# Kernel optimization log

Hardware: AMD Instinct MI355X
Metric: run time of the kernel (lower is better)

The kernel has to match this reference:

```python
import jax, jax.numpy as jnp
import numpy as np
import math

S_SLOTS = 8
DS = 256
ITERS = 3
SIGMA = 5.0
L = 6        # fourier frequencies
FB = 2.0     # freq base
SCALE = DS ** -0.5


def ln(x, g, b, eps=1e-5):
    m = x.mean(-1, keepdims=True)
    v = ((x - m) ** 2).mean(-1, keepdims=True)
    return (x - m) / jnp.sqrt(v + eps) * g + b


def fourier(c):
    # c: (..., 3) -> (..., 3 + 2*3*L), layout [coords, interleaved (sin,cos) per (dim,freq)]
    freqs = FB ** jnp.arange(L, dtype=c.dtype)
    sc = c[..., None] * freqs * (2.0 * math.pi)            # (..., 3, L)
    ff = jnp.stack([jnp.sin(sc), jnp.cos(sc)], axis=-1)    # (..., 3, L, 2)
    ff = ff.reshape(*c.shape[:-1], -1)
    return jnp.concatenate([c, ff], axis=-1)


def n2n(x):
    return jnp.nan_to_num(x, nan=0.0, posinf=1.0, neginf=-1.0)


def gru_cell(x, h, wih, whh, bih, bhh):
    gi = x @ wih.T + bih
    gh = h @ whh.T + bhh
    ir, iz, inn = jnp.split(gi, 3, axis=-1)
    hr, hz, hn = jnp.split(gh, 3, axis=-1)
    r = jax.nn.sigmoid(ir + hr)
    z = jax.nn.sigmoid(iz + hz)
    n = jnp.tanh(inn + r * hn)
    return (1.0 - z) * n + z * h


def isa_forward(inputs, coords, slots_p, Ss0, Sp0, Qw, Kw, Vw, gw, gb,
                f1w, f1b, f2w, f2b, ng, nb, wih, whh, bih, bhh,
                m_ng, m_nb, m1w, m1b, m2w, m2b,
                i0g, i0b, i1w, i1b, i2w, i2b, i3g, i3b, fw, fb):
    B, N, D = inputs.shape
    eps = 1e-8
    slots = jnp.broadcast_to(slots_p, (B, S_SLOTS, DS))
    slots_init = slots
    # initial_mlp: LN -> Linear -> ReLU -> Linear -> LN
    x = ln(inputs, i0g, i0b)
    x = jax.nn.relu(x @ i1w.T + i1b)
    x = x @ i2w.T + i2b
    x = ln(x, i3g, i3b)
    x = n2n(x)                              # (B, N, DS)
    Kx = x @ Kw.T                           # (B, N, DS) (same for every slot)
    Vx = x @ Vw.T
    abs_grid = coords[:, None]              # (B, 1, N, 3)
    S_p = jnp.broadcast_to(Sp0, (B, S_SLOTS, 1, 3))
    S_s = jnp.broadcast_to(Ss0, (B, S_SLOTS, 1, 3))

    def f_mlp(t):
        return jax.nn.relu(t @ f1w.T + f1b) @ f2w.T + f2b

    attn = None
    for t in range(ITERS + 1):
        if t == ITERS - 1:  # query_opt straight-through trick
            slots = jax.lax.stop_gradient(slots) + slots_init - jax.lax.stop_gradient(slots_init)
        slots_prev = slots
        sn = ln(slots, ng, nb)
        Ss_safe = jnp.clip(S_s, 0.3, 5.0) + 0.1
        rel = jnp.clip((abs_grid - S_p) / (Ss_safe * SIGMA + 1e-4), -3.0, 3.0)  # (B,S,N,3)
        gr = fourier(rel) @ gw.T + gb                                           # (B,S,N,DS)
        k = f_mlp(Kx[:, None] + gr)
        v = f_mlp(Vx[:, None] + gr)
        q = sn @ Qw.T                                                           # (B,S,DS)
        dots = jnp.clip(jnp.einsum('bsd,bsnd->bsn', q, k) * SCALE, -30.0, 30.0)
        attn = jax.nn.softmax(dots, axis=1) + eps          # softmax over slots
        attn = attn / (attn.sum(-1, keepdims=True) + eps)  # normalize over points
        updates = jnp.einsum('bsnd,bsn->bsd', v, attn)
        S_p = jnp.einsum('bnd,bsn->bsd', coords, attn)[:, :, None]              # (B,S,1,3)
        diff2 = (abs_grid - S_p) ** 2
        S_s = jnp.clip(jnp.sqrt(jnp.einsum('bsnd,bsn->bsd', diff2, attn) + 1e-6), 0.2, 5.0)[:, :, None]
        if t != ITERS:
            upd = n2n(updates).reshape(-1, DS)
            slots = gru_cell(upd, slots_prev.reshape(-1, DS), wih, whh, bih, bhh).reshape(B, S_SLOTS, DS)
            # pre-norm residual MLP (dropout is identity in eval)
            h = ln(slots, m_ng, m_nb)
            slots = slots + (jax.nn.relu(h @ m1w.T + m1b) @ m2w.T + m2b)
            slots = n2n(slots)
    out_slots = slots_prev @ fw.T + fb
    return out_slots, attn


def setup_inputs() -> dict:
    key = jax.random.key(0)
    ks = iter(jax.random.split(key, 64))
    B, N, D = 4, 2048, 768
    CENC = 3 + 2 * 3 * L  # 39

    def rn(shape, s=0.05):
        return (jax.random.normal(next(ks), shape, jnp.float32) * s)

    d = dict(
        inputs=jax.random.normal(next(ks), (B, N, D), jnp.float32),
        coords=jax.random.uniform(next(ks), (B, N, 3), jnp.float32),
        slots_p=rn((1, S_SLOTS, DS)),
        Ss0=0.5 + 0.1 * jax.random.normal(next(ks), (1, S_SLOTS, 1, 3), jnp.float32),
        Sp0=0.02 * jax.random.normal(next(ks), (1, S_SLOTS, 1, 3), jnp.float32),
        Qw=rn((DS, DS)), Kw=rn((DS, DS)), Vw=rn((DS, DS)),
        gw=rn((DS, CENC)), gb=jnp.zeros((DS,), jnp.float32),
        f1w=rn((DS, DS)), f1b=jnp.zeros((DS,), jnp.float32),
        f2w=rn((DS, DS)), f2b=jnp.zeros((DS,), jnp.float32),
        ng=jnp.ones((DS,), jnp.float32), nb=jnp.zeros((DS,), jnp.float32),
        wih=rn((3 * DS, DS)), whh=rn((3 * DS, DS)),
        bih=jnp.zeros((3 * DS,), jnp.float32), bhh=jnp.zeros((3 * DS,), jnp.float32),
        m_ng=jnp.ones((DS,), jnp.float32), m_nb=jnp.zeros((DS,), jnp.float32),
        m1w=rn((4 * DS, DS)), m1b=jnp.zeros((4 * DS,), jnp.float32),
        m2w=rn((DS, 4 * DS)), m2b=jnp.zeros((DS,), jnp.float32),
        i0g=jnp.ones((D,), jnp.float32), i0b=jnp.zeros((D,), jnp.float32),
        i1w=rn((D, D), 0.03), i1b=jnp.zeros((D,), jnp.float32),
        i2w=rn((DS, D), 0.03), i2b=jnp.zeros((DS,), jnp.float32),
        i3g=jnp.ones((DS,), jnp.float32), i3b=jnp.zeros((DS,), jnp.float32),
        fw=rn((DS, DS)), fb=jnp.zeros((DS,), jnp.float32),
    )
    return d


def reference(inputs, coords, slots_p, Ss0, Sp0, Qw, Kw, Vw, gw, gb,
              f1w, f1b, f2w, f2b, ng, nb, wih, whh, bih, bhh,
              m_ng, m_nb, m1w, m1b, m2w, m2b,
              i0g, i0b, i1w, i1b, i2w, i2b, i3g, i3b, fw, fb):
    return isa_forward(inputs, coords, slots_p, Ss0, Sp0, Qw, Kw, Vw, gw, gb,
                       f1w, f1b, f2w, f2b, ng, nb, wih, whh, bih, bhh,
                       m_ng, m_nb, m1w, m1b, m2w, m2b,
                       i0g, i0b, i1w, i1b, i2w, i2b, i3g, i3b, fw, fb)
```

## Files before the change

kernel.cpp:

```cpp
#include <hip/hip_runtime.h>
#include <math.h>

#define DEVI __device__ __forceinline__

typedef __attribute__((ext_vector_type(8))) short short8;
typedef __attribute__((ext_vector_type(4))) float f32x4;

DEVI float bf2f(short u){ unsigned v = ((unsigned)(unsigned short)u) << 16; return __builtin_bit_cast(float, v); }
DEVI short f2bs(float f){
  unsigned x = __builtin_bit_cast(unsigned, f);
  unsigned r = (x + 0x7fffu + ((x >> 16) & 1u)) >> 16;
  return (short)(unsigned short)r;
}
DEVI float clampf(float x, float lo, float hi){ return fminf(fmaxf(x, lo), hi); }
DEVI float n2nf(float x){
  if (x != x) return 0.f;
  if (x == INFINITY) return 1.f;
  if (x == -INFINITY) return -1.f;
  return x;
}
DEVI float sigmoidf(float x){ return 1.f/(1.f+expf(-x)); }
DEVI f32x4 mfma16(short8 a, short8 b, f32x4 c){ return __builtin_amdgcn_mfma_f32_16x16x32_bf16(a,b,c,0,0,0); }

DEVI float blkSum(float v, float* s4, int tid){
  #pragma unroll
  for (int o=32;o;o>>=1) v += __shfl_xor(v,o);
  __syncthreads();
  if ((tid&63)==0) s4[tid>>6] = v;
  __syncthreads();
  return s4[0]+s4[1]+s4[2]+s4[3];
}

DEVI float ffval(int c, float r0, float r1, float r2){
  if (c >= 40) return 0.f;
  if (c == 39) return 1.f;
  if (c < 3) return (c==0)?r0:((c==1)?r1:r2);
  int q = c-3, i = q/12, j = (q%12)>>1;
  float ri = (i==0)?r0:((i==1)?r1:r2);
  float ang = ri * (6.283185307179586f * (float)(1u<<j));
  return (q&1) ? __cosf(ang) : __sinf(ang);
}

DEVI void qprep_body(float sl, int bs, int t,
    const float* __restrict__ ng, const float* __restrict__ nbv, const float* __restrict__ Qw,
    const float* __restrict__ f2w, const float* __restrict__ f2b,
    float* __restrict__ qf2, float* __restrict__ qbv,
    float* sn, float* q, float* s4){
  float m = blkSum(sl, s4, t)*(1.f/256.f);
  float d = sl - m;
  float var = blkSum(d*d, s4, t)*(1.f/256.f);
  sn[t] = d*(1.f/sqrtf(var+1e-5f))*ng[t] + nbv[t];
  __syncthreads();
  {
    const float4* qr = (const float4*)(Qw + (size_t)t*256);
    float s = 0.f;
    for (int d4=0; d4<64; ++d4){
      float4 w4 = qr[d4];
      s += sn[d4*4+0]*w4.x + sn[d4*4+1]*w4.y + sn[d4*4+2]*w4.z + sn[d4*4+3]*w4.w;
    }
    q[t] = s;
  }
  __syncthreads();
  {
    float s = 0.f;
    for (int o=0;o<256;o++) s += q[o]*f2w[(size_t)o*256 + t];
    qf2[bs*256+t] = s;
  }
  float tot = blkSum(q[t]*f2b[t], s4, t);
  if (t==0) qbv[bs] = tot;
}

__global__ void k_pack_w(const float* __restrict__ W, short* __restrict__ out, int KT, int total){
  int o = blockIdx.x*256 + threadIdx.x;
  if (o >= total) return;
  int l = o & 63;
  int frag = o >> 6;
  int KTt = KT >> 5;
  int ci = frag / KTt, kk = frag - ci*KTt;
  int col = ci*16 + (l & 15);
  int k0 = kk*32 + (l >> 4)*8;
  const float* src = W + (size_t)col*KT + k0;
  short8 v;
  #pragma unroll
  for (int e=0;e<8;e++) v[e] = f2bs(src[e]);
  *(short8*)(out + (size_t)o*8) = v;
}

__global__ void k_pack_gw(const float* __restrict__ gw, const float* __restrict__ gb, short* __restrict__ out){
  int o = blockIdx.x*256 + threadIdx.x;
  int l = o & 63;
  int frag = o >> 6;
  int ci = frag >> 1, kk = frag & 1;
  int col = ci*16 + (l&15);
  int k0 = kk*32 + (l>>4)*8;
  short8 v;
  #pragma unroll
  for (int e=0;e<8;e++){
    int c = k0 + e;
    float x = (c < 39) ? gw[col*39 + c] : (c == 39 ? gb[col] : 0.f);
    v[e] = f2bs(x);
  }
  *(short8*)(out + (size_t)o*8) = v;
}

__global__ __launch_bounds__(256) void k_init(const float* __restrict__ slots_p, const float* __restrict__ Sp0,
                       const float* __restrict__ Ss0,
                       float* __restrict__ slots, float* __restrict__ sp, float* __restrict__ ssb,
                       const float* __restrict__ ng, const float* __restrict__ nbv, const float* __restrict__ Qw,
                       const float* __restrict__ f2w, const float* __restrict__ f2b,
                       float* __restrict__ qf2, float* __restrict__ qbv){
  int bs = blockIdx.x, t = threadIdx.x, s = bs & 7;
  __shared__ float sn[256], q[256], s4[4];
  float sl = slots_p[s*256+t];
  slots[bs*256+t] = sl;
  if (t < 3){ sp[bs*3+t] = Sp0[s*3+t]; ssb[bs*3+t] = Ss0[s*3+t]; }
  qprep_body(sl, bs, t, ng, nbv, Qw, f2w, f2b, qf2, qbv, sn, q, s4);
}

__global__ __launch_bounds__(256) void k_ln768(const float* __restrict__ in, const float* __restrict__ g,
                                               const float* __restrict__ bt, short* __restrict__ out){
  int r = blockIdx.x, t = threadIdx.x;
  __shared__ float s4[4];
  const float* row = in + (size_t)r*768;
  float x0=row[t], x1=row[256+t], x2=row[512+t];
  float m = blkSum(x0+x1+x2, s4, t) * (1.f/768.f);
  float d0=x0-m, d1=x1-m, d2=x2-m;
  float var = blkSum(d0*d0+d1*d1+d2*d2, s4, t) * (1.f/768.f);
  float rstd = 1.f/sqrtf(var + 1e-5f);
  short* orow = out + (size_t)r*768;
  orow[t]     = f2bs(d0*rstd*g[t]     + bt[t]);
  orow[256+t] = f2bs(d1*rstd*g[256+t] + bt[256+t]);
  orow[512+t] = f2bs(d2*rstd*g[512+t] + bt[512+t]);
}

__global__ __launch_bounds__(256) void k_ln256(const float* __restrict__ in, const float* __restrict__ g,
                                               const float* __restrict__ bt, short* __restrict__ out){
  int r = blockIdx.x, t = threadIdx.x;
  __shared__ float s4[4];
  float x = in[(size_t)r*256 + t];
  float m = blkSum(x, s4, t) * (1.f/256.f);
  float d = x - m;
  float var = blkSum(d*d, s4, t) * (1.f/256.f);
  out[(size_t)r*256 + t] = f2bs(d*(1.f/sqrtf(var+1e-5f))*g[t] + bt[t]);
}

__global__ __launch_bounds__(256) void k_gemm(const short* __restrict__ A, const short* __restrict__ Wp,
                                              const float* __restrict__ bias, void* __restrict__ outp,
                                              int ldo, int KT, int flags){
  const int w = threadIdx.x>>6, l = threadIdx.x&63, l15 = l&15, l4 = l>>4;
  const int row0 = blockIdx.x*64 + w*16;
  const int col0 = blockIdx.y*128;
  const int KTt = KT >> 5;
  f32x4 acc[8];
  #pragma unroll
  for (int i=0;i<8;i++) acc[i] = (f32x4)(0.f);
  const short* Ap = A + (size_t)(row0+l15)*KT + l4*8;
  #pragma unroll 2
  for (int kk=0; kk<KT/32; ++kk){
    short8 af = *(const short8*)(Ap + kk*32);
    #pragma unroll
    for (int ci=0; ci<8; ++ci){
      const short* bp = Wp + (((size_t)(blockIdx.y*8+ci)*KTt + kk)*64 + l)*8;
      acc[ci] = mfma16(af, *(const short8*)bp, acc[ci]);
    }
  }
  #pragma unroll
  for (int ci=0; ci<8; ++ci){
    int col = col0 + ci*16 + l15;
    float bv = (flags&1) ? bias[col] : 0.f;
    #pragma unroll
    for (int j=0;j<4;j++){
      int row = row0 + l4*4 + j;
      float v = acc[ci][j] + bv;
      if (flags&2) v = fmaxf(v, 0.f);
      if (flags&4) ((short*)outp)[(size_t)row*ldo + col] = f2bs(v);
      else         ((float*)outp)[(size_t)row*ldo + col] = v;
    }
  }
}

__global__ __launch_bounds__(256, 4) void k_isa_a(
    const float* __restrict__ coords, const float* __restrict__ sp, const float* __restrict__ ssb,
    const short* __restrict__ gwp, const short* __restrict__ kx, const short* __restrict__ vx,
    const short* __restrict__ f1wp, const float* __restrict__ f1b,
    const float* __restrict__ qf2, const float* __restrict__ qbv,
    float* __restrict__ dots, short* __restrict__ hv){
  __shared__ __align__(16) short abuf[64*256];
  __shared__ float sf1b[256];
  __shared__ float sqf2[256];
  __shared__ float smisc[8];
  const int tid = threadIdx.x;
  const int bs = blockIdx.y;
  const int b  = bs >> 3;
  const int n0 = blockIdx.x * 64;
  const int pass = blockIdx.z;

  sf1b[tid] = f1b[tid];
  sqf2[tid] = qf2[bs*256 + tid];
  if (tid < 3){
    smisc[tid] = sp[bs*3+tid];
    float sv = ssb[bs*3+tid];
    float sa = clampf(sv, 0.3f, 5.f) + 0.1f;
    smisc[4+tid] = 1.f/(sa*5.f + 1e-4f);
  }
  if (tid == 7) smisc[7] = qbv[bs];
  __syncthreads();

  const int w = tid>>6, l = tid&63, l15 = l&15, l4 = l>>4;
  const int ar = w*16 + l15;

  short8 ag0, ag1;
  {
    const float* cp0 = coords + ((size_t)(b*2048 + n0 + ar))*3;
    float r0 = clampf((cp0[0] - smisc[0]) * smisc[4], -3.f, 3.f);
    float r1 = clampf((cp0[1] - smisc[1]) * smisc[5], -3.f, 3.f);
    float r2 = clampf((cp0[2] - smisc[2]) * smisc[6], -3.f, 3.f);
    #pragma unroll
    for (int e=0;e<8;e++) ag0[e] = f2bs(ffval(l4*8+e,      r0,r1,r2));
    #pragma unroll
    for (int e=0;e<8;e++) ag1[e] = f2bs(ffval(32+l4*8+e,   r0,r1,r2));
  }

  #pragma unroll 2
  for (int cc=0; cc<8; ++cc){
    int f0 = (2*cc)*2, f1 = (2*cc+1)*2;
    f32x4 a0 = (f32x4)(0.f), a1 = (f32x4)(0.f);
    a0 = mfma16(ag0, *(const short8*)(gwp + ((size_t)(f0  )*64 + l)*8), a0);
    a0 = mfma16(ag1, *(const short8*)(gwp + ((size_t)(f0+1)*64 + l)*8), a0);
    a1 = mfma16(ag0, *(const short8*)(gwp + ((size_t)(f1  )*64 + l)*8), a1);
    a1 = mfma16(ag1, *(const short8*)(gwp + ((size_t)(f1+1)*64 + l)*8), a1);
    int c0 = (2*cc)*16 + l15, c1 = (2*cc+1)*16 + l15;
    #pragma unroll
    for (int j=0;j<4;j++){
      int row = w*16 + l4*4 + j;
      abuf[row*256 + (((c0>>3)^(row&7))<<3) + (c0&7)] = f2bs(a0[j]);
      abuf[row*256 + (((c1>>3)^(row&7))<<3) + (c1&7)] = f2bs(a1[j]);
    }
  }
  __syncthreads();
  {
    const short* srcb = pass ? vx : kx;
    #pragma unroll
    for (int i=0;i<8;i++){
      int gid = tid + i*256;
      int row = gid>>5, cg = gid&31;
      short8 sv = *(const short8*)(srcb + ((size_t)(b*2048 + n0 + row))*256 + cg*8);
      short* ap = &abuf[row*256 + ((cg^(row&7))<<3)];
      short8 av = *(const short8*)ap;
      short8 ov;
      #pragma unroll
      for (int e=0;e<8;e++) ov[e] = f2bs(bf2f(av[e]) + bf2f(sv[e]));
      *(short8*)ap = ov;
    }
  }
  __syncthreads();
  short8 af[8];
  #pragma unroll
  for (int kk=0;kk<8;kk++)
    af[kk] = *(const short8*)&abuf[ar*256 + (((kk*4+l4) ^ (ar&7))<<3)];

  if (pass == 0){
    float p0=0.f,p1=0.f,p2=0.f,p3=0.f;
    #pragma unroll 2
    for (int cc=0; cc<8; ++cc){
      int ct0 = 2*cc, ct1 = 2*cc+1;
      f32x4 a0 = (f32x4)(0.f), a1 = (f32x4)(0.f);
      #pragma unroll
      for (int kk=0;kk<8;kk++){
        a0 = mfma16(af[kk], *(const short8*)(f1wp + (((size_t)ct0*8 + kk)*64 + l)*8), a0);
        a1 = mfma16(af[kk], *(const short8*)(f1wp + (((size_t)ct1*8 + kk)*64 + l)*8), a1);
      }
      int c0 = ct0*16 + l15, c1 = ct1*16 + l15;
      float q0=sqf2[c0], b0=sf1b[c0], q1=sqf2[c1], b1=sf1b[c1];
      p0 += fmaxf(a0[0]+b0,0.f)*q0 + fmaxf(a1[0]+b1,0.f)*q1;
      p1 += fmaxf(a0[1]+b0,0.f)*q0 + fmaxf(a1[1]+b1,0.f)*q1;
      p2 += fmaxf(a0[2]+b0,0.f)*q0 + fmaxf(a1[2]+b1,0.f)*q1;
      p3 += fmaxf(a0[3]+b0,0.f)*q0 + fmaxf(a1[3]+b1,0.f)*q1;
    }
    #pragma unroll
    for (int o=8;o;o>>=1){
      p0 += __shfl_xor(p0,o); p1 += __shfl_xor(p1,o);
      p2 += __shfl_xor(p2,o); p3 += __shfl_xor(p3,o);
    }
    if (l15 == 0){
      float pj[4] = {p0,p1,p2,p3};
      #pragma unroll
      for (int j=0;j<4;j++){
        int row = w*16 + l4*4 + j;
        float dd = clampf((pj[j] + smisc[7]) * 0.0625f, -30.f, 30.f);
        dots[(size_t)bs*2048 + n0 + row] = dd;
      }
    }
  } else {
    #pragma unroll 2
    for (int cc=0; cc<8; ++cc){
      int ct0 = 2*cc, ct1 = 2*cc+1;
      f32x4 a0 = (f32x4)(0.f), a1 = (f32x4)(0.f);
      #pragma unroll
      for (int kk=0;kk<8;kk++){
        a0 = mfma16(af[kk], *(const short8*)(f1wp + (((size_t)ct0*8 + kk)*64 + l)*8), a0);
        a1 = mfma16(af[kk], *(const short8*)(f1wp + (((size_t)ct1*8 + kk)*64 + l)*8), a1);
      }
      int c0 = ct0*16 + l15, c1 = ct1*16 + l15;
      float b0=sf1b[c0], b1=sf1b[c1];
      #pragma unroll
      for (int j=0;j<4;j++){
        int row = w*16 + l4*4 + j;
        abuf[row*256 + (((c0>>3)^(row&7))<<3) + (c0&7)] = f2bs(fmaxf(a0[j]+b0,0.f));
        abuf[row*256 + (((c1>>3)^(row&7))<<3) + (c1&7)] = f2bs(fmaxf(a1[j]+b1,0.f));
      }
    }
    __syncthreads();
    #pragma unroll
    for (int i=0;i<8;i++){
      int gid = tid + i*256;
      int row = gid>>5, cg = gid&31;
      short8 av = *(const short8*)&abuf[row*256 + ((cg^(row&7))<<3)];
      *(short8*)(hv + ((size_t)(bs*2048 + n0 + row))*256 + cg*8) = av;
    }
  }
}

__global__ __launch_bounds__(256) void k_softmax(const float* __restrict__ dots, float* __restrict__ aun,
                                                 float* __restrict__ sump){
  int blk = blockIdx.x;
  int b = blk >> 3, chunk = blk & 7;
  int n = chunk*256 + threadIdx.x;
  float d[8];
  #pragma unroll
  for (int s=0;s<8;s++) d[s] = dots[(size_t)(b*8+s)*2048 + n];
  float m = d[0];
  #pragma unroll
  for (int s=1;s<8;s++) m = fmaxf(m, d[s]);
  float e[8]; float sum = 0.f;
  #pragma unroll
  for (int s=0;s<8;s++){ e[s] = expf(d[s]-m); sum += e[s]; }
  float inv = 1.f/sum;
  __shared__ float red[4][8];
  int wv = threadIdx.x>>6, ln = threadIdx.x&63;
  #pragma unroll
  for (int s=0;s<8;s++){
    float a = e[s]*inv + 1e-8f;
    aun[(size_t)(b*8+s)*2048 + n] = a;
    float v = a;
    #pragma unroll
    for (int o=32;o;o>>=1) v += __shfl_xor(v,o);
    if (ln == 0) red[wv][s] = v;
  }
  __syncthreads();
  if (threadIdx.x < 8){
    int s = threadIdx.x;
    sump[(b*8+s)*8 + chunk] = red[0][s]+red[1][s]+red[2][s]+red[3][s];
  }
}

__global__ __launch_bounds__(256) void k_c1(const float* __restrict__ dots, const short* __restrict__ hv,
    const float* __restrict__ coords, float* __restrict__ hvpart, float* __restrict__ mompart,
    float* __restrict__ sump){
  int chunk = blockIdx.x, bs = blockIdx.y, b = bs >> 3, so = bs & 7;
  int t = threadIdx.x;
  int nb = chunk*256;
  __shared__ float wsm[256];
  {
    float d[8];
    #pragma unroll
    for (int s=0;s<8;s++) d[s] = dots[(size_t)(b*8+s)*2048 + nb + t];
    float m = d[0];
    #pragma unroll
    for (int s=1;s<8;s++) m = fmaxf(m, d[s]);
    float sum = 0.f; float eo = 0.f;
    #pragma unroll
    for (int s=0;s<8;s++){ float e = expf(d[s]-m); sum += e; if (s==so) eo = e; }
    wsm[t] = eo/sum + 1e-8f;
  }
  __syncthreads();
  float acc = 0.f;
  const short* hp = hv + ((size_t)bs*2048 + nb)*256 + t;
  #pragma unroll 4
  for (int n=0;n<256;n++) acc += wsm[n]*bf2f(hp[(size_t)n*256]);
  hvpart[(size_t)(bs*8+chunk)*256 + t] = acc;
  float wv = wsm[t];
  const float* cp = coords + ((size_t)(b*2048) + nb + t)*3;
  float c0=cp[0], c1=cp[1], c2=cp[2];
  float mv[7] = {wv*c0, wv*c1, wv*c2, wv*c0*c0, wv*c1*c1, wv*c2*c2, wv};
  __shared__ float red[4][7];
  int wvx = t>>6, ln = t&63;
  #pragma unroll
  for (int i=0;i<7;i++){
    float v = mv[i];
    #pragma unroll
    for (int o=32;o;o>>=1) v += __shfl_xor(v,o);
    if (ln==0) red[wvx][i] = v;
  }
  __syncthreads();
  if (t<7){
    float r = red[0][t]+red[1][t]+red[2][t]+red[3][t];
    if (t<6) mompart[(bs*8+chunk)*6 + t] = r;
    else     sump[bs*8 + chunk] = r;
  }
}

__global__ __launch_bounds__(256) void k_c2(
    const float* __restrict__ hvpart, const float* __restrict__ mompart, const float* __restrict__ sump,
    const float* __restrict__ f2w, const float* __restrict__ f2b,
    float* __restrict__ sp, float* __restrict__ ssb,
    const float* __restrict__ wih, const float* __restrict__ whh,
    const float* __restrict__ bih, const float* __restrict__ bhh,
    const float* __restrict__ m_ng, const float* __restrict__ m_nb,
    const float* __restrict__ m1w, const float* __restrict__ m1b,
    const float* __restrict__ m2w, const float* __restrict__ m2b,
    float* __restrict__ slots,
    const float* __restrict__ ng, const float* __restrict__ nbv, const float* __restrict__ Qw,
    float* __restrict__ qf2, float* __restrict__ qbv){
  int bs = blockIdx.x, t = threadIdx.x;
  __shared__ float hs[256], u[256], spv[256], hln[256], r1[1024];
  __shared__ float sc[8], s4[4];
  {
    float a=0.f;
    #pragma unroll
    for (int c=0;c<8;c++) a += hvpart[(size_t)(bs*8+c)*256 + t];
    hs[t] = a;
  }
  spv[t] = slots[bs*256+t];
  if (t == 0){
    float A0=0.f;
    for (int c=0;c<8;c++) A0 += sump[bs*8+c];
    sc[0]=A0; sc[1]=A0+1e-8f;
  }
  if (t < 6){
    float mm=0.f;
    for (int c=0;c<8;c++) mm += mompart[(bs*8+c)*6 + t];
    sc[2+t] = mm;
  }
  __syncthreads();
  float A0 = sc[0], denom = sc[1];
  if (t < 3){
    float A1 = sc[2+t], A2 = sc[5+t];
    float p = A1/denom;
    float var = (A2 - 2.f*p*A1 + p*p*A0)/denom + 1e-6f;
    float sv = clampf(sqrtf(var), 0.2f, 5.f);
    sp[bs*3+t] = p; ssb[bs*3+t] = sv;
  }
  {
    float dd = 0.f;
    const float4* fr = (const float4*)(f2w + (size_t)t*256);
    for (int h4=0; h4<64; ++h4){
      float4 w4 = fr[h4];
      dd += hs[h4*4+0]*w4.x + hs[h4*4+1]*w4.y + hs[h4*4+2]*w4.z + hs[h4*4+3]*w4.w;
    }
    u[t] = n2nf((dd + A0*f2b[t])/denom);
  }
  __syncthreads();
  float gi[3], gh[3];
  #pragma unroll 1
  for (int part=0; part<3; ++part){
    int o = part*256 + t;
    const float4* wr = (const float4*)(wih + (size_t)o*256);
    const float4* hr = (const float4*)(whh + (size_t)o*256);
    float si = bih[o], sh = bhh[o];
    for (int d4=0; d4<64; ++d4){
      float4 a4 = wr[d4], b4 = hr[d4];
      si += u[d4*4+0]*a4.x + u[d4*4+1]*a4.y + u[d4*4+2]*a4.z + u[d4*4+3]*a4.w;
      sh += spv[d4*4+0]*b4.x + spv[d4*4+1]*b4.y + spv[d4*4+2]*b4.z + spv[d4*4+3]*b4.w;
    }
    gi[part]=si; gh[part]=sh;
  }
  float rg = sigmoidf(gi[0]+gh[0]);
  float zg = sigmoidf(gi[1]+gh[1]);
  float nn = tanhf(gi[2] + rg*gh[2]);
  float hnew = (1.f-zg)*nn + zg*spv[t];
  float m = blkSum(hnew, s4, t)*(1.f/256.f);
  float dv = hnew - m;
  float var = blkSum(dv*dv, s4, t)*(1.f/256.f);
  hln[t] = dv*(1.f/sqrtf(var+1e-5f))*m_ng[t] + m_nb[t];
  __syncthreads();
  #pragma unroll 1
  for (int oi=0; oi<4; ++oi){
    int o = t*4 + oi;
    const float4* mr = (const float4*)(m1w + (size_t)o*256);
    float s = m1b[o];
    for (int d4=0; d4<64; ++d4){
      float4 a4 = mr[d4];
      s += hln[d4*4+0]*a4.x + hln[d4*4+1]*a4.y + hln[d4*4+2]*a4.z + hln[d4*4+3]*a4.w;
    }
    r1[o] = fmaxf(s, 0.f);
  }
  __syncthreads();
  float sl;
  {
    const float4* mr = (const float4*)(m2w + (size_t)t*1024);
    float s = m2b[t];
    for (int o4=0; o4<256; ++o4){
      float4 a4 = mr[o4];
      s += r1[o4*4+0]*a4.x + r1[o4*4+1]*a4.y + r1[o4*4+2]*a4.z + r1[o4*4+3]*a4.w;
    }
    sl = n2nf(hnew + s);
    slots[bs*256+t] = sl;
  }
  qprep_body(sl, bs, t, ng, nbv, Qw, f2w, f2b, qf2, qbv, hs, u, s4);
}

__global__ __launch_bounds__(256) void k_attn_out(const float* __restrict__ aun, const float* __restrict__ sump,
                                                  float* __restrict__ outp){
  int g = blockIdx.x*256 + threadIdx.x;
  int bs = g >> 11;
  __shared__ float dsh;
  if (threadIdx.x == 0){
    float s=0.f;
    for (int c=0;c<8;c++) s += sump[bs*8+c];
    dsh = s + 1e-8f;
  }
  __syncthreads();
  outp[g] = aun[g] / dsh;
}

__global__ __launch_bounds__(256) void k_final(const float* __restrict__ slots,
    const float* __restrict__ fw, const float* __restrict__ fb, float* __restrict__ outp){
  int bs = blockIdx.x, t = threadIdx.x;
  __shared__ float sl[256];
  sl[t] = slots[bs*256+t];
  __syncthreads();
  const float4* fr = (const float4*)(fw + (size_t)t*256);
  float s = fb[t];
  for (int d4=0; d4<64; ++d4){
    float4 w4 = fr[d4];
    s += sl[d4*4+0]*w4.x + sl[d4*4+1]*w4.y + sl[d4*4+2]*w4.z + sl[d4*4+3]*w4.w;
  }
  outp[bs*256+t] = s;
}

extern "C" void kernel_launch(void* const* d_in, const int* in_sizes, int n_in,
                              void* d_out, int out_size, void* d_ws, size_t ws_size,
                              hipStream_t stream){
  const float* p_inputs = (const float*)d_in[0];
  const float* p_coords = (const float*)d_in[1];
  const float* p_slotsp = (const float*)d_in[2];
  const float* p_Ss0 = (const float*)d_in[3];
  const float* p_Sp0 = (const float*)d_in[4];
  const float* p_Qw  = (const float*)d_in[5];
  const float* p_Kw  = (const float*)d_in[6];
  const float* p_Vw  = (const float*)d_in[7];
  const float* p_gw  = (const float*)d_in[8];
  const float* p_gb  = (const float*)d_in[9];
  const float* p_f1w = (const float*)d_in[10];
  const float* p_f1b = (const float*)d_in[11];
  const float* p_f2w = (const float*)d_in[12];
  const float* p_f2b = (const float*)d_in[13];
  const float* p_ng  = (const float*)d_in[14];
  const float* p_nb  = (const float*)d_in[15];
  const float* p_wih = (const float*)d_in[16];
  const float* p_whh = (const float*)d_in[17];
  const float* p_bih = (const float*)d_in[18];
  const float* p_bhh = (const float*)d_in[19];
  const float* p_mng = (const float*)d_in[20];
  const float* p_mnb = (const float*)d_in[21];
  const float* p_m1w = (const float*)d_in[22];
  const float* p_m1b = (const float*)d_in[23];
  const float* p_m2w = (const float*)d_in[24];
  const float* p_m2b = (const float*)d_in[25];
  const float* p_i0g = (const float*)d_in[26];
  const float* p_i0b = (const float*)d_in[27];
  const float* p_i1w = (const float*)d_in[28];
  const float* p_i1b = (const float*)d_in[29];
  const float* p_i2w = (const float*)d_in[30];
  const float* p_i2b = (const float*)d_in[31];
  const float* p_i3g = (const float*)d_in[32];
  const float* p_i3b = (const float*)d_in[33];
  const float* p_fw  = (const float*)d_in[34];
  const float* p_fb  = (const float*)d_in[35];

  char* ws = (char*)d_ws;
  size_t off = 0;
  auto alloc = [&](size_t bytes)->char*{
    char* p = ws + off;
    off = (off + bytes + 255) & ~(size_t)255;
    return p;
  };
  short* xln   = (short*)alloc(8192ull*768*2);
  short* h1    = (short*)alloc(8192ull*768*2);
  float* x2    = (float*)alloc(8192ull*256*4);
  short* xenc  = (short*)alloc(8192ull*256*2);
  short* kxb   = (short*)alloc(8192ull*256*2);
  short* vxb   = (short*)alloc(8192ull*256*2);
  short* hvb   = (short*)alloc(32ull*2048*256*2);
  float* dots  = (float*)alloc(32ull*2048*4);
  float* aun   = (float*)alloc(32ull*2048*4);
  float* sump  = (float*)alloc(32*8*4);
  float* hvpart= (float*)alloc(32ull*8*256*4);
  float* mompart=(float*)alloc(32*8*6*4);
  short* i1wp  = (short*)alloc(768ull*768*2);
  short* i2wp  = (short*)alloc(256ull*768*2);
  short* kwp   = (short*)alloc(256ull*256*2);
  short* vwp   = (short*)alloc(256ull*256*2);
  short* f1wp  = (short*)alloc(256ull*256*2);
  short* gwp   = (short*)alloc(256ull*64*2);
  float* slots = (float*)alloc(32*256*4);
  float* qf2   = (float*)alloc(32*256*4);
  float* qbv   = (float*)alloc(32*4);
  float* spb   = (float*)alloc(32*3*4);
  float* ssbuf = (float*)alloc(32*3*4);

  k_pack_w<<<(768*768/8+255)/256,256,0,stream>>>(p_i1w, i1wp, 768, 768*768/8);
  k_pack_w<<<(256*768/8+255)/256,256,0,stream>>>(p_i2w, i2wp, 768, 256*768/8);
  k_pack_w<<<(256*256/8+255)/256,256,0,stream>>>(p_Kw,  kwp,  256, 256*256/8);
  k_pack_w<<<(256*256/8+255)/256,256,0,stream>>>(p_Vw,  vwp,  256, 256*256/8);
  k_pack_w<<<(256*256/8+255)/256,256,0,stream>>>(p_f1w, f1wp, 256, 256*256/8);
  k_pack_gw<<<8,256,0,stream>>>(p_gw, p_gb, gwp);
  k_init<<<32,256,0,stream>>>(p_slotsp, p_Sp0, p_Ss0, slots, spb, ssbuf,
                              p_ng, p_nb, p_Qw, p_f2w, p_f2b, qf2, qbv);

  k_ln768<<<8192,256,0,stream>>>(p_inputs, p_i0g, p_i0b, xln);
  k_gemm<<<dim3(128,6),256,0,stream>>>(xln, i1wp, p_i1b, h1, 768, 768, 1|2|4);
  k_gemm<<<dim3(128,2),256,0,stream>>>(h1, i2wp, p_i2b, x2, 256, 768, 1);
  k_ln256<<<8192,256,0,stream>>>(x2, p_i3g, p_i3b, xenc);
  k_gemm<<<dim3(128,2),256,0,stream>>>(xenc, kwp, nullptr, kxb, 256, 256, 4);
  k_gemm<<<dim3(128,2),256,0,stream>>>(xenc, vwp, nullptr, vxb, 256, 256, 4);

  float* outf = (float*)d_out;
  for (int t=0;t<4;t++){
    k_isa_a<<<dim3(32,32,(t<3)?2:1),256,0,stream>>>(p_coords, spb, ssbuf, gwp, kxb, vxb, f1wp, p_f1b, qf2, qbv, dots, hvb);
    if (t < 3){
      k_c1<<<dim3(8,32),256,0,stream>>>(dots, hvb, p_coords, hvpart, mompart, sump);
      k_c2<<<32,256,0,stream>>>(hvpart, mompart, sump, p_f2w, p_f2b, spb, ssbuf,
                                p_wih, p_whh, p_bih, p_bhh, p_mng, p_mnb,
                                p_m1w, p_m1b, p_m2w, p_m2b, slots,
                                p_ng, p_nb, p_Qw, qf2, qbv);
    } else {
      k_softmax<<<32,256,0,stream>>>(dots, aun, sump);
      k_attn_out<<<256,256,0,stream>>>(aun, sump, outf + 8192);
    }
  }
  k_final<<<32,256,0,stream>>>(slots, p_fw, p_fb, outf);
}
```

Baseline: 843.7 us.

## Widen slot-update kernel to 1024 threads with bf16 weights and transposed f2w

The per-slot update kernel (GRU, MLP, LN, Q projection) now runs with 1024 threads per block instead of 256. Matrix-vector products are split into four K-slices and reduced through shared memory. GRU and MLP weights are pre-converted to bf16 to halve their load bytes, and f2w is pre-transposed so qprep reads it coalesced along rows. The weighted reduction in k_c1 now stages hv rows through an LDS tile with short8 loads. The trade-offs are extra setup kernels, more barriers, and bf16 rounding of the GRU and MLP weights.

```diff
diff --git a/kernel.cpp b/kernel.cpp
--- a/kernel.cpp
+++ b/kernel.cpp
@@ -43,7 +43,7 @@
 
 DEVI void qprep_body(float sl, int bs, int t,
     const float* __restrict__ ng, const float* __restrict__ nbv, const float* __restrict__ Qw,
-    const float* __restrict__ f2w, const float* __restrict__ f2b,
+    const float* __restrict__ f2wT, const float* __restrict__ f2b,
     float* __restrict__ qf2, float* __restrict__ qbv,
     float* sn, float* q, float* s4){
   float m = blkSum(sl, s4, t)*(1.f/256.f);
@@ -62,12 +62,26 @@
   }
   __syncthreads();
   {
+    const float4* fr = (const float4*)(f2wT + (size_t)t*256);
     float s = 0.f;
-    for (int o=0;o<256;o++) s += q[o]*f2w[(size_t)o*256 + t];
+    for (int d4=0; d4<64; ++d4){
+      float4 w4 = fr[d4];
+      s += q[d4*4+0]*w4.x + q[d4*4+1]*w4.y + q[d4*4+2]*w4.z + q[d4*4+3]*w4.w;
+    }
     qf2[bs*256+t] = s;
   }
   float tot = blkSum(q[t]*f2b[t], s4, t);
   if (t==0) qbv[bs] = tot;
+}
+
+__global__ void k_convert(const float* __restrict__ s, short* __restrict__ d, int n){
+  int i = blockIdx.x*256 + threadIdx.x;
+  if (i < n) d[i] = f2bs(s[i]);
+}
+
+__global__ void k_transpose256(const float* __restrict__ in, float* __restrict__ out){
+  int c = blockIdx.x, r = threadIdx.x;
+  out[(size_t)c*256 + r] = in[(size_t)r*256 + c];
 }
 
 __global__ void k_pack_w(const float* __restrict__ W, short* __restrict__ out, int KT, int total){
@@ -107,14 +121,14 @@
                        const float* __restrict__ Ss0,
                        float* __restrict__ slots, float* __restrict__ sp, float* __restrict__ ssb,
                        const float* __restrict__ ng, const float* __restrict__ nbv, const float* __restrict__ Qw,
-                       const float* __restrict__ f2w, const float* __restrict__ f2b,
+                       const float* __restrict__ f2wT, const float* __restrict__ f2b,
                        float* __restrict__ qf2, float* __restrict__ qbv){
   int bs = blockIdx.x, t = threadIdx.x, s = bs & 7;
   __shared__ float sn[256], q[256], s4[4];
   float sl = slots_p[s*256+t];
   slots[bs*256+t] = sl;
   if (t < 3){ sp[bs*3+t] = Sp0[s*3+t]; ssb[bs*3+t] = Ss0[s*3+t]; }
-  qprep_body(sl, bs, t, ng, nbv, Qw, f2w, f2b, qf2, qbv, sn, q, s4);
+  qprep_body(sl, bs, t, ng, nbv, Qw, f2wT, f2b, qf2, qbv, sn, q, s4);
 }
 
 __global__ __launch_bounds__(256) void k_ln768(const float* __restrict__ in, const float* __restrict__ g,
@@ -361,6 +375,7 @@
   int t = threadIdx.x;
   int nb = chunk*256;
   __shared__ float wsm[256];
+  __shared__ __align__(16) short tile[16*256];
   {
     float d[8];
     #pragma unroll
@@ -375,9 +390,21 @@
   }
   __syncthreads();
   float acc = 0.f;
-  const short* hp = hv + ((size_t)bs*2048 + nb)*256 + t;
-  #pragma unroll 4
-  for (int n=0;n<256;n++) acc += wsm[n]*bf2f(hp[(size_t)n*256]);
+  const short* hbase = hv + ((size_t)bs*2048 + nb)*256;
+  #pragma unroll 1
+  for (int c16=0; c16<16; ++c16){
+    #pragma unroll
+    for (int rep=0; rep<2; ++rep){
+      int idx = t + rep*256;
+      int r = idx>>5, cg = idx&31;
+      *(short8*)&tile[r*256 + cg*8] = *(const short8*)(hbase + (size_t)(c16*16+r)*256 + cg*8);
+    }
+    __syncthreads();
+    #pragma unroll 4
+    for (int n2=0;n2<16;n2++)
+      acc += wsm[c16*16+n2]*bf2f(tile[n2*256+t]);
+    __syncthreads();
+  }
   hvpart[(size_t)(bs*8+chunk)*256 + t] = acc;
   float wv = wsm[t];
   const float* cp = coords + ((size_t)(b*2048) + nb + t)*3;
@@ -400,104 +427,193 @@
   }
 }
 
-__global__ __launch_bounds__(256) void k_c2(
+__global__ __launch_bounds__(1024) void k_c2(
     const float* __restrict__ hvpart, const float* __restrict__ mompart, const float* __restrict__ sump,
     const float* __restrict__ f2w, const float* __restrict__ f2b,
     float* __restrict__ sp, float* __restrict__ ssb,
-    const float* __restrict__ wih, const float* __restrict__ whh,
+    const short* __restrict__ wihp, const short* __restrict__ whhp,
     const float* __restrict__ bih, const float* __restrict__ bhh,
     const float* __restrict__ m_ng, const float* __restrict__ m_nb,
-    const float* __restrict__ m1w, const float* __restrict__ m1b,
-    const float* __restrict__ m2w, const float* __restrict__ m2b,
+    const short* __restrict__ m1wp, const float* __restrict__ m1b,
+    const short* __restrict__ m2wp, const float* __restrict__ m2b,
     float* __restrict__ slots,
     const float* __restrict__ ng, const float* __restrict__ nbv, const float* __restrict__ Qw,
+    const float* __restrict__ f2wT,
     float* __restrict__ qf2, float* __restrict__ qbv){
   int bs = blockIdx.x, t = threadIdx.x;
+  int lo = t & 255, grp = t >> 8;
   __shared__ float hs[256], u[256], spv[256], hln[256], r1[1024];
-  __shared__ float sc[8], s4[4];
-  {
-    float a=0.f;
-    #pragma unroll
-    for (int c=0;c<8;c++) a += hvpart[(size_t)(bs*8+c)*256 + t];
-    hs[t] = a;
-  }
-  spv[t] = slots[bs*256+t];
+  __shared__ float gis[768], ghs[768];
+  __shared__ float red4[4][256];
+  __shared__ float sc[8], rtmp[8];
+
+  red4[grp][lo] = hvpart[(size_t)(bs*8+grp*2)*256+lo] + hvpart[(size_t)(bs*8+grp*2+1)*256+lo];
+  if (t < 256) spv[lo] = slots[bs*256+lo];
   if (t == 0){
     float A0=0.f;
     for (int c=0;c<8;c++) A0 += sump[bs*8+c];
     sc[0]=A0; sc[1]=A0+1e-8f;
   }
-  if (t < 6){
+  if (t >= 64 && t < 70){
+    int i = t-64;
     float mm=0.f;
-    for (int c=0;c<8;c++) mm += mompart[(bs*8+c)*6 + t];
-    sc[2+t] = mm;
-  }
-  __syncthreads();
-  float A0 = sc[0], denom = sc[1];
+    for (int c=0;c<8;c++) mm += mompart[(bs*8+c)*6 + i];
+    sc[2+i] = mm;
+  }
+  __syncthreads();
+  if (t < 256) hs[lo] = red4[0][lo]+red4[1][lo]+red4[2][lo]+red4[3][lo];
   if (t < 3){
+    float A0=sc[0], denom=sc[1];
     float A1 = sc[2+t], A2 = sc[5+t];
     float p = A1/denom;
     float var = (A2 - 2.f*p*A1 + p*p*A0)/denom + 1e-6f;
-    float sv = clampf(sqrtf(var), 0.2f, 5.f);
-    sp[bs*3+t] = p; ssb[bs*3+t] = sv;
-  }
-  {
+    sp[bs*3+t] = p; ssb[bs*3+t] = clampf(sqrtf(var),0.2f,5.f);
+  }
+  __syncthreads();
+  {
+    const float4* fr = (const float4*)(f2w + (size_t)lo*256 + grp*64);
+    const float* hsp = hs + grp*64;
     float dd = 0.f;
-    const float4* fr = (const float4*)(f2w + (size_t)t*256);
-    for (int h4=0; h4<64; ++h4){
-      float4 w4 = fr[h4];
-      dd += hs[h4*4+0]*w4.x + hs[h4*4+1]*w4.y + hs[h4*4+2]*w4.z + hs[h4*4+3]*w4.w;
-    }
-    u[t] = n2nf((dd + A0*f2b[t])/denom);
-  }
-  __syncthreads();
-  float gi[3], gh[3];
-  #pragma unroll 1
-  for (int part=0; part<3; ++part){
-    int o = part*256 + t;
-    const float4* wr = (const float4*)(wih + (size_t)o*256);
-    const float4* hr = (const float4*)(whh + (size_t)o*256);
-    float si = bih[o], sh = bhh[o];
-    for (int d4=0; d4<64; ++d4){
-      float4 a4 = wr[d4], b4 = hr[d4];
-      si += u[d4*4+0]*a4.x + u[d4*4+1]*a4.y + u[d4*4+2]*a4.z + u[d4*4+3]*a4.w;
-      sh += spv[d4*4+0]*b4.x + spv[d4*4+1]*b4.y + spv[d4*4+2]*b4.z + spv[d4*4+3]*b4.w;
-    }
-    gi[part]=si; gh[part]=sh;
-  }
-  float rg = sigmoidf(gi[0]+gh[0]);
-  float zg = sigmoidf(gi[1]+gh[1]);
-  float nn = tanhf(gi[2] + rg*gh[2]);
-  float hnew = (1.f-zg)*nn + zg*spv[t];
-  float m = blkSum(hnew, s4, t)*(1.f/256.f);
-  float dv = hnew - m;
-  float var = blkSum(dv*dv, s4, t)*(1.f/256.f);
-  hln[t] = dv*(1.f/sqrtf(var+1e-5f))*m_ng[t] + m_nb[t];
-  __syncthreads();
-  #pragma unroll 1
-  for (int oi=0; oi<4; ++oi){
-    int o = t*4 + oi;
-    const float4* mr = (const float4*)(m1w + (size_t)o*256);
-    float s = m1b[o];
-    for (int d4=0; d4<64; ++d4){
-      float4 a4 = mr[d4];
-      s += hln[d4*4+0]*a4.x + hln[d4*4+1]*a4.y + hln[d4*4+2]*a4.z + hln[d4*4+3]*a4.w;
-    }
-    r1[o] = fmaxf(s, 0.f);
-  }
-  __syncthreads();
-  float sl;
-  {
-    const float4* mr = (const float4*)(m2w + (size_t)t*1024);
-    float s = m2b[t];
-    for (int o4=0; o4<256; ++o4){
-      float4 a4 = mr[o4];
-      s += r1[o4*4+0]*a4.x + r1[o4*4+1]*a4.y + r1[o4*4+2]*a4.z + r1[o4*4+3]*a4.w;
-    }
-    sl = n2nf(hnew + s);
-    slots[bs*256+t] = sl;
-  }
-  qprep_body(sl, bs, t, ng, nbv, Qw, f2w, f2b, qf2, qbv, hs, u, s4);
+    #pragma unroll 4
+    for (int i=0;i<16;i++){
+      float4 w4 = fr[i];
+      dd += hsp[i*4+0]*w4.x + hsp[i*4+1]*w4.y + hsp[i*4+2]*w4.z + hsp[i*4+3]*w4.w;
+    }
+    red4[grp][lo] = dd;
+  }
+  __syncthreads();
+  if (t < 256)
+    u[lo] = n2nf((red4[0][lo]+red4[1][lo]+red4[2][lo]+red4[3][lo] + sc[0]*f2b[lo])/sc[1]);
+  __syncthreads();
+  if (t < 768){
+    const short8* wr = (const short8*)(wihp + (size_t)t*256);
+    const short8* hr = (const short8*)(whhp + (size_t)t*256);
+    float si = bih[t], sh = bhh[t];
+    #pragma unroll 4
+    for (int i=0;i<32;i++){
+      short8 a = wr[i], b8 = hr[i];
+      #pragma unroll
+      for (int e=0;e<8;e++){
+        si += u[i*8+e]*bf2f(a[e]);
+        sh += spv[i*8+e]*bf2f(b8[e]);
+      }
+    }
+    gis[t]=si; ghs[t]=sh;
+  }
+  __syncthreads();
+  float hnewv = 0.f;
+  if (t < 256){
+    float rg = sigmoidf(gis[lo]+ghs[lo]);
+    float zg = sigmoidf(gis[256+lo]+ghs[256+lo]);
+    float nn = tanhf(gis[512+lo] + rg*ghs[512+lo]);
+    hnewv = (1.f-zg)*nn + zg*spv[lo];
+    red4[0][lo] = hnewv;
+  }
+  __syncthreads();
+  if (t < 64){
+    float s = red4[0][t]+red4[0][t+64]+red4[0][t+128]+red4[0][t+192];
+    #pragma unroll
+    for (int o=32;o;o>>=1) s += __shfl_xor(s,o);
+    if (t==0) rtmp[0] = s*(1.f/256.f);
+  }
+  __syncthreads();
+  if (t < 64){
+    float m = rtmp[0], s=0.f;
+    #pragma unroll
+    for (int i=0;i<4;i++){ float d = red4[0][t+64*i]-m; s += d*d; }
+    #pragma unroll
+    for (int o=32;o;o>>=1) s += __shfl_xor(s,o);
+    if (t==0) rtmp[1] = s*(1.f/256.f);
+  }
+  __syncthreads();
+  if (t < 256)
+    hln[lo] = (hnewv - rtmp[0])*(1.f/sqrtf(rtmp[1]+1e-5f))*m_ng[lo] + m_nb[lo];
+  __syncthreads();
+  {
+    const short8* mr = (const short8*)(m1wp + (size_t)t*256);
+    float s = m1b[t];
+    #pragma unroll 4
+    for (int i=0;i<32;i++){
+      short8 a = mr[i];
+      #pragma unroll
+      for (int e=0;e<8;e++) s += hln[i*8+e]*bf2f(a[e]);
+    }
+    r1[t] = fmaxf(s, 0.f);
+  }
+  __syncthreads();
+  {
+    const short8* mr = (const short8*)(m2wp + (size_t)lo*1024 + grp*256);
+    const float* rp = r1 + grp*256;
+    float s = 0.f;
+    #pragma unroll 4
+    for (int i=0;i<32;i++){
+      short8 a = mr[i];
+      #pragma unroll
+      for (int e=0;e<8;e++) s += rp[i*8+e]*bf2f(a[e]);
+    }
+    red4[grp][lo] = s;
+  }
+  __syncthreads();
+  float sl = 0.f;
+  if (t < 256){
+    sl = n2nf(hnewv + m2b[lo] + red4[0][lo]+red4[1][lo]+red4[2][lo]+red4[3][lo]);
+    slots[bs*256+lo] = sl;
+    red4[0][lo] = sl;
+  }
+  __syncthreads();
+  if (t < 64){
+    float s = red4[0][t]+red4[0][t+64]+red4[0][t+128]+red4[0][t+192];
+    #pragma unroll
+    for (int o=32;o;o>>=1) s += __shfl_xor(s,o);
+    if (t==0) rtmp[2] = s*(1.f/256.f);
+  }
+  __syncthreads();
+  if (t < 64){
+    float m = rtmp[2], s=0.f;
+    #pragma unroll
+    for (int i=0;i<4;i++){ float d = red4[0][t+64*i]-m; s += d*d; }
+    #pragma unroll
+    for (int o=32;o;o>>=1) s += __shfl_xor(s,o);
+    if (t==0) rtmp[3] = s*(1.f/256.f);
+  }
+  __syncthreads();
+  if (t < 256)
+    hs[lo] = (sl - rtmp[2])*(1.f/sqrtf(rtmp[3]+1e-5f))*ng[lo] + nbv[lo];
+  __syncthreads();
+  {
+    const float4* qr = (const float4*)(Qw + (size_t)lo*256 + grp*64);
+    const float* snp = hs + grp*64;
+    float s = 0.f;
+    #pragma unroll 4
+    for (int i=0;i<16;i++){
+      float4 w4 = qr[i];
+      s += snp[i*4+0]*w4.x + snp[i*4+1]*w4.y + snp[i*4+2]*w4.z + snp[i*4+3]*w4.w;
+    }
+    red4[grp][lo] = s;
+  }
+  __syncthreads();
+  if (t < 256) u[lo] = red4[0][lo]+red4[1][lo]+red4[2][lo]+red4[3][lo];
+  __syncthreads();
+  {
+    const float4* fr = (const float4*)(f2wT + (size_t)lo*256 + grp*64);
+    const float* qp = u + grp*64;
+    float s = 0.f;
+    #pragma unroll 4
+    for (int i=0;i<16;i++){
+      float4 w4 = fr[i];
+      s += qp[i*4+0]*w4.x + qp[i*4+1]*w4.y + qp[i*4+2]*w4.z + qp[i*4+3]*w4.w;
+    }
+    red4[grp][lo] = s;
+  }
+  __syncthreads();
+  if (t < 256)
+    qf2[bs*256+lo] = red4[0][lo]+red4[1][lo]+red4[2][lo]+red4[3][lo];
+  if (t < 64){
+    float s = u[t]*f2b[t] + u[t+64]*f2b[t+64] + u[t+128]*f2b[t+128] + u[t+192]*f2b[t+192];
+    #pragma unroll
+    for (int o=32;o;o>>=1) s += __shfl_xor(s,o);
+    if (t==0) qbv[bs] = s;
+  }
 }
 
 __global__ __launch_bounds__(256) void k_attn_out(const float* __restrict__ aun, const float* __restrict__ sump,
@@ -594,20 +710,33 @@
   short* vwp   = (short*)alloc(256ull*256*2);
   short* f1wp  = (short*)alloc(256ull*256*2);
   short* gwp   = (short*)alloc(256ull*64*2);
+  short* wihp  = (short*)alloc(768ull*256*2);
+  short* whhp  = (short*)alloc(768ull*256*2);
+  short* m1wp  = (short*)alloc(1024ull*256*2);
+  short* m2wp  = (short*)alloc(256ull*1024*2);
+  float* f2wT  = (float*)alloc(256ull*256*4);
   float* slots = (float*)alloc(32*256*4);
   float* qf2   = (float*)alloc(32*256*4);
   float* qbv   = (float*)alloc(32*4);
   float* spb   = (float*)alloc(32*3*4);
   float* ssbuf = (float*)alloc(32*3*4);
 
+  auto cvt = [&](const float* s, short* dst, int n){
+    k_convert<<<(n+255)/256, 256, 0, stream>>>(s, dst, n);
+  };
   k_pack_w<<<(768*768/8+255)/256,256,0,stream>>>(p_i1w, i1wp, 768, 768*768/8);
   k_pack_w<<<(256*768/8+255)/256,256,0,stream>>>(p_i2w, i2wp, 768, 256*768/8);
   k_pack_w<<<(256*256/8+255)/256,256,0,stream>>>(p_Kw,  kwp,  256, 256*256/8);
   k_pack_w<<<(256*256/8+255)/256,256,0,stream>>>(p_Vw,  vwp,  256, 256*256/8);
   k_pack_w<<<(256*256/8+255)/256,256,0,stream>>>(p_f1w, f1wp, 256, 256*256/8);
   k_pack_gw<<<8,256,0,stream>>>(p_gw, p_gb, gwp);
+  cvt(p_wih, wihp, 768*256);
+  cvt(p_whh, whhp, 768*256);
+  cvt(p_m1w, m1wp, 1024*256);
+  cvt(p_m2w, m2wp, 256*1024);
+  k_transpose256<<<256,256,0,stream>>>(p_f2w, f2wT);
   k_init<<<32,256,0,stream>>>(p_slotsp, p_Sp0, p_Ss0, slots, spb, ssbuf,
-                              p_ng, p_nb, p_Qw, p_f2w, p_f2b, qf2, qbv);
+                              p_ng, p_nb, p_Qw, f2wT, p_f2b, qf2, qbv);
 
   k_ln768<<<8192,256,0,stream>>>(p_inputs, p_i0g, p_i0b, xln);
   k_gemm<<<dim3(128,6),256,0,stream>>>(xln, i1wp, p_i1b, h1, 768, 768, 1|2|4);
@@ -621,10 +750,10 @@
     k_isa_a<<<dim3(32,32,(t<3)?2:1),256,0,stream>>>(p_coords, spb, ssbuf, gwp, kxb, vxb, f1wp, p_f1b, qf2, qbv, dots, hvb);
     if (t < 3){
       k_c1<<<dim3(8,32),256,0,stream>>>(dots, hvb, p_coords, hvpart, mompart, sump);
-      k_c2<<<32,256,0,stream>>>(hvpart, mompart, sump, p_f2w, p_f2b, spb, ssbuf,
-                                p_wih, p_whh, p_bih, p_bhh, p_mng, p_mnb,
-                                p_m1w, p_m1b, p_m2w, p_m2b, slots,
-                                p_ng, p_nb, p_Qw, qf2, qbv);
+      k_c2<<<32,1024,0,stream>>>(hvpart, mompart, sump, p_f2w, p_f2b, spb, ssbuf,
+                                 wihp, whhp, p_bih, p_bhh, p_mng, p_mnb,
+                                 m1wp, p_m1b, m2wp, p_m2b, slots,
+                                 p_ng, p_nb, p_Qw, f2wT, qf2, qbv);
     } else {
       k_softmax<<<32,256,0,stream>>>(dots, aun, sump);
       k_attn_out<<<256,256,0,stream>>>(aun, sump, outf + 8192);
```

Result: faster. 700.2 us (-17.0%).
